# Optimization experiments

Measured on AMD Instinct MI355X. Metric: run time of the kernel, lower is better.

The kernel has to match this reference:

```python
import jax, jax.numpy as jnp
import numpy as np

N = 200_000          # nodes
E = 6_400_000        # edges (avg degree 32)
U, T, C, G = 200_000, 20_000, 5_000, 10_000  # table sizes
DU, DT, DC, DG = 8, 8, 2, 8                  # embedding dims
IC, H, OC = 8, 16, 1                          # input/hidden/output channels


def setup_inputs() -> dict:
    key = jax.random.key(0)
    ks = jax.random.split(key, 24)
    # node type in {0,1,2,4}
    tcode = jnp.array([0, 1, 2, 4], dtype=jnp.int32)[jax.random.randint(ks[0], (N,), 0, 4)]
    # per-type in-range index (size lookup by type code; slot 3 unused)
    sizes = jnp.array([U, T, C, 1, G], dtype=jnp.float32)
    u = jax.random.uniform(ks[1], (N,))
    idx = jnp.floor(u * sizes[tcode]).astype(jnp.int32)
    known = jax.random.randint(ks[2], (N,), 0, 2).astype(jnp.int32)
    features = jnp.stack([idx, known, tcode], axis=1)  # [N, 3]
    edges = jax.random.randint(ks[3], (2, E), 0, N).astype(jnp.int32)
    label_masks = jax.random.randint(ks[4], (N,), 0, 2).astype(jnp.int32)

    def w(k, shape, s=0.1):
        return jax.random.normal(k, shape, dtype=jnp.float32) * s

    return {
        "edges": edges, "features": features, "label_masks": label_masks,
        "user_emb": w(ks[5], (U, DU)), "known_emb": w(ks[6], (2, DU)),
        "mask_emb": w(ks[7], (2, DU)), "cat_emb": w(ks[8], (C, DC)),
        "topic_emb": w(ks[9], (T, DT)), "group_emb": w(ks[10], (G, DG)),
        "user_W": w(ks[11], (DU, IC)), "user_b": jnp.zeros((IC,), jnp.float32),
        "mask_W": w(ks[12], (DU, IC)), "mask_b": jnp.zeros((IC,), jnp.float32),
        "cat_W": w(ks[13], (DC, IC)), "cat_b": jnp.zeros((IC,), jnp.float32),
        "topic_W": w(ks[14], (DT, IC)), "topic_b": jnp.zeros((IC,), jnp.float32),
        "group_W": w(ks[15], (DG, IC)), "group_b": jnp.zeros((IC,), jnp.float32),
        "W0": w(ks[16], (IC, H)), "b0": jnp.zeros((H,), jnp.float32),
        "W2": w(ks[17], (H, OC)), "b2": jnp.zeros((OC,), jnp.float32),
    }


def _assemble(features, label_masks, user_emb, known_emb, mask_emb, cat_emb,
              topic_emb, group_emb, user_W, user_b, mask_W, mask_b, cat_W, cat_b,
              topic_W, topic_b, group_W, group_b):
    idx, known, tcode = features[:, 0], features[:, 1], features[:, 2]
    relu = jax.nn.relu
    # proj = Sequential(ReLU, Linear): relu first, then linear
    user_f = relu(user_emb[jnp.clip(idx, 0, U - 1)] + known_emb[jnp.clip(known, 0, 1)]) @ user_W + user_b
    topic_f = relu(topic_emb[jnp.clip(idx, 0, T - 1)]) @ topic_W + topic_b
    cat_f = relu(cat_emb[jnp.clip(idx, 0, C - 1)]) @ cat_W + cat_b
    group_f = relu(group_emb[jnp.clip(idx, 0, G - 1)]) @ group_W + group_b
    t = tcode[:, None]
    x = jnp.where(t == 0, user_f,
        jnp.where(t == 1, topic_f,
        jnp.where(t == 2, cat_f,
        jnp.where(t == 4, group_f, 0.0))))
    mask_f = jax.nn.sigmoid(relu(mask_emb[label_masks]) @ mask_W + mask_b)
    return x * mask_f  # [N, IC]


def _gcn_norm(edges, n):
    # add self-loops, symmetric normalization (PyG GCNConv default)
    loops = jnp.arange(n, dtype=edges.dtype)
    row = jnp.concatenate([edges[0], loops])
    col = jnp.concatenate([edges[1], loops])
    deg = jax.ops.segment_sum(jnp.ones_like(col, dtype=jnp.float32), col, num_segments=n)
    dis = jnp.where(deg > 0, jax.lax.rsqrt(jnp.where(deg > 0, deg, 1.0)), 0.0)
    return row, col, dis[row] * dis[col]


def _gcn_conv(x, row, col, norm, W, b):
    h = x @ W                                   # [N, out]
    msg = norm[:, None] * h[row]                # gather + scale over edges
    out = jax.ops.segment_sum(msg, col, num_segments=x.shape[0])
    return out + b


def reference(edges, features, label_masks, user_emb, known_emb, mask_emb,
              cat_emb, topic_emb, group_emb, user_W, user_b, mask_W, mask_b,
              cat_W, cat_b, topic_W, topic_b, group_W, group_b, W0, b0, W2, b2):
    x = _assemble(features, label_masks, user_emb, known_emb, mask_emb, cat_emb,
                  topic_emb, group_emb, user_W, user_b, mask_W, mask_b, cat_W,
                  cat_b, topic_W, topic_b, group_W, group_b)
    row, col, norm = _gcn_norm(edges, x.shape[0])
    # Original forward applies layers[0] (relu) then layers[-1]; layers[1] is skipped.
    x = jax.nn.relu(_gcn_conv(x, row, col, norm, W0, b0))
    return _gcn_conv(x, row, col, norm, W2, b2)  # [N, 1]
```

## Files before the change

### kernel.cpp

```cpp
#include <hip/hip_runtime.h>
#include <math.h>

constexpr int NN = 200000;
constexpr int EE = 6400000;
constexpr int NB = (NN + 255) / 256;
constexpr int U_ = 200000, T_ = 20000, C_ = 5000, G_ = 10000;

constexpr int BSH2  = 9;
constexpr int BUCKN = 1 << BSH2;
constexpr int NBUCK = (NN + BUCKN - 1) / BUCKN;
constexpr int CAP   = 18432;
constexpr int CHUNK  = 8192;
constexpr int NCHUNK = (EE + CHUNK - 1) / CHUNK;
constexpr int PER    = (NCHUNK + 255) / 256;

__device__ __forceinline__ int clampi(int v, int lo, int hi){ return v < lo ? lo : (v > hi ? hi : v); }
__device__ __forceinline__ float reluf(float v){ return v > 0.f ? v : 0.f; }


__global__ __launch_bounds__(512) void k_hist(const int* __restrict__ edges,
                                              int* __restrict__ cntmat){
  __shared__ int h[NBUCK];
  int t = threadIdx.x;
  for (int i = t; i < NBUCK; i += 512) h[i] = 0;
  __syncthreads();
  int base = blockIdx.x * CHUNK;
  int n = min(CHUNK, EE - base);
  for (int k = t; k < n; k += 512)
    atomicAdd(&h[edges[EE + base + k] >> BSH2], 1);
  __syncthreads();
  for (int i = t; i < NBUCK; i += 512)
    cntmat[(size_t)blockIdx.x * NBUCK + i] = h[i];
}


__global__ void k_scan2(const int* __restrict__ cntmat, int* __restrict__ offT,
                        int* __restrict__ binCnt){
  __shared__ int sc[256];
  int t = threadIdx.x;
  int b = blockIdx.x;
  int v[PER];
  int loc = 0;
  #pragma unroll
  for (int j = 0; j < PER; j++){
    int c = t * PER + j;
    v[j] = (c < NCHUNK) ? cntmat[(size_t)c * NBUCK + b] : 0;
    loc += v[j];
  }
  sc[t] = loc; __syncthreads();
  for (int d = 1; d < 256; d <<= 1){
    int u = (t >= d) ? sc[t - d] : 0;
    __syncthreads();
    sc[t] += u;
    __syncthreads();
  }
  int run = b * CAP + sc[t] - loc;
  #pragma unroll
  for (int j = 0; j < PER; j++){
    int c = t * PER + j;
    if (c < NCHUNK){ offT[(size_t)b * NCHUNK + c] = run; run += v[j]; }
  }
  if (t == 255) binCnt[b] = sc[255];
}


__global__ __launch_bounds__(512) void k_binA3(const int* __restrict__ edges,
                                               const int* __restrict__ cntmat,
                                               const int* __restrict__ offT,
                                               int* __restrict__ bin){
  __shared__ int cur[NBUCK];
  __shared__ int dlt[NBUCK];
  __shared__ int wsum[8];
  __shared__ int stage[CHUNK];
  __shared__ unsigned short stageB[CHUNK];

  int t = threadIdx.x;
  int chunk = blockIdx.x;
  int my = (t < NBUCK) ? cntmat[(size_t)chunk * NBUCK + t] : 0;
  int lane = t & 63, wid = t >> 6;
  int incl = my;
  #pragma unroll
  for (int d = 1; d < 64; d <<= 1){
    int u = __shfl_up(incl, d);
    if (lane >= d) incl += u;
  }
  if (lane == 63) wsum[wid] = incl;
  __syncthreads();
  int wpre = 0;
  #pragma unroll
  for (int w = 0; w < 8; w++) wpre += (w < wid) ? wsum[w] : 0;
  int excl = wpre + incl - my;
  if (t < NBUCK){
    cur[t] = excl;
    dlt[t] = offT[(size_t)t * NCHUNK + chunk] - excl;
  }
  __syncthreads();
  int base = chunk * CHUNK;
  int n = min(CHUNK, EE - base);
  for (int k = t; k < n; k += 512){
    int c = edges[EE + base + k];
    int r = edges[base + k];
    int b = c >> BSH2;
    int p = atomicAdd(&cur[b], 1);
    stage[p]  = r | ((c & (BUCKN - 1)) << 18);
    stageB[p] = (unsigned short)b;
  }
  __syncthreads();
  for (int k = t; k < n; k += 512){
    int b = stageB[k];
    int addr = dlt[b] + k;
    if (addr < (b + 1) * CAP)
      bin[addr] = stage[k];
  }
}


__global__ __launch_bounds__(512) void k_binB2(
    const int* __restrict__ bin, const int* __restrict__ binCnt,
    int* __restrict__ off, int* __restrict__ deg, int* __restrict__ seg,
    double* __restrict__ dis, int* __restrict__ srow){
  __shared__ int hist[4 * BUCKN];
  __shared__ int sc[512];
  int t = threadIdx.x;
  int b = blockIdx.x;
  int nb = b << BSH2;
  int nloc = min(BUCKN, NN - nb);
  int s0 = b * CAP;
  int s1 = s0 + min(binCnt[b], CAP);

  hist[t] = 0; hist[t + 512] = 0; hist[t + 1024] = 0; hist[t + 1536] = 0;
  __syncthreads();
  for (int k = s0 + t; k < s1; k += 512){
    int w = bin[k];
    int key = ((w >> 18) << 2) | ((w & 0x3FFFF) >> 16);
    atomicAdd(&hist[key], 1);
  }
  __syncthreads();
  int h0 = hist[4*t], h1 = hist[4*t+1], h2 = hist[4*t+2], h3 = hist[4*t+3];
  int tot = h0 + h1 + h2 + h3;
  sc[t] = tot; __syncthreads();
  for (int d = 1; d < 512; d <<= 1){
    int u = (t >= d) ? sc[t - d] : 0;
    __syncthreads();
    sc[t] += u;
    __syncthreads();
  }
  int base = sc[t] - tot;
  if (t < nloc){
    off[nb + t] = s0 + base;
    deg[nb + t] = tot;
    seg[nb + t] = h0 | ((h0 + h1) << 10) | ((h0 + h1 + h2) << 20);
    dis[nb + t] = 1.0 / sqrt((double)(tot + 1));
  }
  __syncthreads();
  hist[4*t]     = base;
  hist[4*t + 1] = base + h0;
  hist[4*t + 2] = base + h0 + h1;
  hist[4*t + 3] = base + h0 + h1 + h2;
  __syncthreads();
  for (int k = s0 + t; k < s1; k += 512){
    int w = bin[k];
    int key = ((w >> 18) << 2) | ((w & 0x3FFFF) >> 16);
    int p = atomicAdd(&hist[key], 1);
    srow[s0 + p] = w & 0x3FFFF;
  }
}


__global__ void k_assemble(
    const int* __restrict__ features, const int* __restrict__ lmask,
    const float* __restrict__ user_emb, const float* __restrict__ known_emb,
    const float* __restrict__ mask_emb, const float* __restrict__ cat_emb,
    const float* __restrict__ topic_emb, const float* __restrict__ group_emb,
    const float* __restrict__ user_W, const float* __restrict__ user_b,
    const float* __restrict__ mask_W, const float* __restrict__ mask_b,
    const float* __restrict__ cat_W, const float* __restrict__ cat_b,
    const float* __restrict__ topic_W, const float* __restrict__ topic_b,
    const float* __restrict__ group_W, const float* __restrict__ group_b,
    const double* __restrict__ dis, float* __restrict__ xs1)
{
  __shared__ float s_userW[64], s_topicW[64], s_groupW[64], s_maskW[64];
  __shared__ float s_catW[16], s_knownE[16], s_maskE[16];
  __shared__ float s_userb[8], s_topicb[8], s_catb[8], s_groupb[8], s_maskb[8];
  int tid = threadIdx.x;
  if (tid < 64){ s_userW[tid]=user_W[tid]; s_topicW[tid]=topic_W[tid];
                 s_groupW[tid]=group_W[tid]; s_maskW[tid]=mask_W[tid]; }
  if (tid < 16){ s_catW[tid]=cat_W[tid]; s_knownE[tid]=known_emb[tid]; s_maskE[tid]=mask_emb[tid]; }
  if (tid < 8){ s_userb[tid]=user_b[tid]; s_topicb[tid]=topic_b[tid]; s_catb[tid]=cat_b[tid];
                s_groupb[tid]=group_b[tid]; s_maskb[tid]=mask_b[tid]; }
  __syncthreads();

  int i = blockIdx.x * 256 + tid;
  if (i >= NN) return;

  int idx   = features[3*i + 0];
  int known = features[3*i + 1];
  int tc    = features[3*i + 2];

  double x[8];
  #pragma unroll
  for (int k = 0; k < 8; k++) x[k] = 0.0;

  if (tc == 0){
    int id = clampi(idx, 0, U_-1);
    int kn = clampi(known, 0, 1);
    float a[8];
    #pragma unroll
    for (int d = 0; d < 8; d++) a[d] = reluf(user_emb[(size_t)id*8 + d] + s_knownE[kn*8 + d]);
    #pragma unroll
    for (int k = 0; k < 8; k++){
      double s = (double)s_userb[k];
      #pragma unroll
      for (int d = 0; d < 8; d++) s += (double)a[d] * (double)s_userW[d*8 + k];
      x[k] = s;
    }
  } else if (tc == 1){
    int id = clampi(idx, 0, T_-1);
    float a[8];
    #pragma unroll
    for (int d = 0; d < 8; d++) a[d] = reluf(topic_emb[(size_t)id*8 + d]);
    #pragma unroll
    for (int k = 0; k < 8; k++){
      double s = (double)s_topicb[k];
      #pragma unroll
      for (int d = 0; d < 8; d++) s += (double)a[d] * (double)s_topicW[d*8 + k];
      x[k] = s;
    }
  } else if (tc == 2){
    int id = clampi(idx, 0, C_-1);
    float a0 = reluf(cat_emb[(size_t)id*2 + 0]);
    float a1 = reluf(cat_emb[(size_t)id*2 + 1]);
    #pragma unroll
    for (int k = 0; k < 8; k++)
      x[k] = (double)s_catb[k] + (double)a0*(double)s_catW[k] + (double)a1*(double)s_catW[8 + k];
  } else if (tc == 4){
    int id = clampi(idx, 0, G_-1);
    float a[8];
    #pragma unroll
    for (int d = 0; d < 8; d++) a[d] = reluf(group_emb[(size_t)id*8 + d]);
    #pragma unroll
    for (int k = 0; k < 8; k++){
      double s = (double)s_groupb[k];
      #pragma unroll
      for (int d = 0; d < 8; d++) s += (double)a[d] * (double)s_groupW[d*8 + k];
      x[k] = s;
    }
  }

  int m = clampi(lmask[i], 0, 1);
  float me[8];
  #pragma unroll
  for (int d = 0; d < 8; d++) me[d] = reluf(s_maskE[m*8 + d]);
  double di = dis[i];
  float xo[8];
  #pragma unroll
  for (int k = 0; k < 8; k++){
    double s = (double)s_maskb[k];
    #pragma unroll
    for (int d = 0; d < 8; d++) s += (double)me[d] * (double)s_maskW[d*8 + k];
    double mf = 1.0 / (1.0 + exp(-s));
    xo[k] = (float)(di * x[k] * mf);
  }
  float4* xp = (float4*)(xs1 + (size_t)i * 8);
  xp[0] = make_float4(xo[0], xo[1], xo[2], xo[3]);
  xp[1] = make_float4(xo[4], xo[5], xo[6], xo[7]);
}


__global__ void k_agg1(const float* __restrict__ xs1, const int* __restrict__ srow,
                       const int* __restrict__ off, const int* __restrict__ cnt,
                       const int* __restrict__ seg, const double* __restrict__ dis,
                       const float* __restrict__ b0, const float* __restrict__ W0,
                       const float* __restrict__ W2, float* __restrict__ h2s)
{
  __shared__ float sW0[128], sb0[16], sW2[16];
  int tid = threadIdx.x;
  if (tid < 128) sW0[tid] = W0[tid];
  if (tid < 16){ sb0[tid] = b0[tid]; sW2[tid] = W2[tid]; }
  __syncthreads();

  int gid = blockIdx.x * 256 + tid;
  int i = gid >> 1, h = gid & 1;
  if (i >= NN) return;

  const float4* xp = (const float4*)xs1;
  float4 sv = xp[(size_t)i*2 + h];
  double a0 = sv.x, a1 = sv.y, a2 = sv.z, a3 = sv.w;
  int s = off[i], c = cnt[i], sg = seg[i];
  int bnd[5];
  bnd[0] = 0;
  bnd[1] = sg & 1023;
  bnd[2] = (sg >> 10) & 1023;
  bnd[3] = (sg >> 20) & 1023;
  bnd[4] = c;
  #pragma unroll 1
  for (int p = 0; p < 4; p++){
    int j = bnd[p], je = bnd[p + 1];
    for (; j + 4 <= je; j += 4){
      int r0 = srow[s+j], r1 = srow[s+j+1], r2 = srow[s+j+2], r3 = srow[s+j+3];
      float4 v0 = xp[(size_t)r0*2 + h], v1 = xp[(size_t)r1*2 + h],
             v2 = xp[(size_t)r2*2 + h], v3 = xp[(size_t)r3*2 + h];
      a0 += v0.x; a1 += v0.y; a2 += v0.z; a3 += v0.w;
      a0 += v1.x; a1 += v1.y; a2 += v1.z; a3 += v1.w;
      a0 += v2.x; a1 += v2.y; a2 += v2.z; a3 += v2.w;
      a0 += v3.x; a1 += v3.y; a2 += v3.z; a3 += v3.w;
    }
    for (; j < je; ++j){
      int r = srow[s + j];
      float4 v = xp[(size_t)r*2 + h];
      a0 += v.x; a1 += v.y; a2 += v.z; a3 += v.w;
    }
  }
  double e0 = __shfl_xor(a0, 1), e1 = __shfl_xor(a1, 1),
         e2 = __shfl_xor(a2, 1), e3 = __shfl_xor(a3, 1);
  double X[8];
  if (h == 0){ X[0]=a0; X[1]=a1; X[2]=a2; X[3]=a3; X[4]=e0; X[5]=e1; X[6]=e2; X[7]=e3; }
  else       { X[0]=e0; X[1]=e1; X[2]=e2; X[3]=e3; X[4]=a0; X[5]=a1; X[6]=a2; X[7]=a3; }

  double di = dis[i];
  double h2p = 0.0;
  #pragma unroll
  for (int jj = 0; jj < 8; jj++){
    int j = h * 8 + jj;
    double t = 0.0;
    #pragma unroll
    for (int cc = 0; cc < 8; cc++) t += X[cc] * (double)sW0[cc*16 + j];
    t = di * t + (double)sb0[j];
    double x2 = t > 0.0 ? t : 0.0;
    h2p += x2 * (double)sW2[j];
  }
  double h2 = h2p + __shfl_xor(h2p, 1);
  if (h == 0) h2s[i] = (float)(di * h2);
}


__global__ void k_agg2(const float* __restrict__ h2s, const int* __restrict__ srow,
                       const int* __restrict__ off, const int* __restrict__ cnt,
                       const double* __restrict__ dis, const float* __restrict__ b2,
                       float* __restrict__ out)
{
  int gid = blockIdx.x * 256 + threadIdx.x;
  int i = gid >> 1, h = gid & 1;
  if (i >= NN) return;
  double acc = (h == 0) ? (double)h2s[i] : 0.0;
  int s = off[i], c = cnt[i];
  for (int j = h; j < c; j += 2)
    acc += (double)h2s[srow[s + j]];
  acc += __shfl_xor(acc, 1);
  if (h == 0) out[i] = (float)(dis[i] * acc + (double)b2[0]);
}


extern "C" void kernel_launch(void* const* d_in, const int* in_sizes, int n_in,
                              void* d_out, int out_size, void* d_ws, size_t ws_size,
                              hipStream_t stream)
{
  const int*   edges      = (const int*)  d_in[0];
  const int*   features   = (const int*)  d_in[1];
  const int*   label_mask = (const int*)  d_in[2];
  const float* user_emb   = (const float*)d_in[3];
  const float* known_emb  = (const float*)d_in[4];
  const float* mask_emb   = (const float*)d_in[5];
  const float* cat_emb    = (const float*)d_in[6];
  const float* topic_emb  = (const float*)d_in[7];
  const float* group_emb  = (const float*)d_in[8];
  const float* user_W     = (const float*)d_in[9];
  const float* user_b     = (const float*)d_in[10];
  const float* mask_W     = (const float*)d_in[11];
  const float* mask_b     = (const float*)d_in[12];
  const float* cat_W      = (const float*)d_in[13];
  const float* cat_b      = (const float*)d_in[14];
  const float* topic_W    = (const float*)d_in[15];
  const float* topic_b    = (const float*)d_in[16];
  const float* group_W    = (const float*)d_in[17];
  const float* group_b    = (const float*)d_in[18];
  const float* W0         = (const float*)d_in[19];
  const float* b0         = (const float*)d_in[20];
  const float* W2         = (const float*)d_in[21];
  const float* b2         = (const float*)d_in[22];
  float* out = (float*)d_out;

  char* ws = (char*)d_ws;
  size_t o = 0;
  auto alloc = [&](size_t bytes){ void* p = ws + o; o += (bytes + 255) & ~255ull; return p; };
  int*    cntmat = (int*)   alloc((size_t)NCHUNK * NBUCK * 4);
  int*    offT   = (int*)   alloc((size_t)NBUCK * NCHUNK * 4);
  int*    binCnt = (int*)   alloc((size_t)NBUCK * 4);
  int*    off    = (int*)   alloc((size_t)NN * 4);
  int*    deg    = (int*)   alloc((size_t)NN * 4);
  int*    seg    = (int*)   alloc((size_t)NN * 4);
  double* dis    = (double*)alloc((size_t)NN * 8);
  int*    srow   = (int*)   alloc((size_t)NBUCK * CAP * 4);
  int*    bin    = (int*)   alloc((size_t)NBUCK * CAP * 4);
  float*  xs1    = (float*) alloc((size_t)NN * 8 * 4);
  float*  h2s    = (float*) alloc((size_t)NN * 4);

  k_hist    <<<NCHUNK, 512, 0, stream>>>(edges, cntmat);
  k_scan2   <<<NBUCK,  256, 0, stream>>>(cntmat, offT, binCnt);
  k_binA3   <<<NCHUNK, 512, 0, stream>>>(edges, cntmat, offT, bin);
  k_binB2   <<<NBUCK,  512, 0, stream>>>(bin, binCnt, off, deg, seg, dis, srow);
  k_assemble<<<NB,     256, 0, stream>>>(features, label_mask,
      user_emb, known_emb, mask_emb, cat_emb, topic_emb, group_emb,
      user_W, user_b, mask_W, mask_b, cat_W, cat_b,
      topic_W, topic_b, group_W, group_b, dis, xs1);
  k_agg1    <<<(2*NN + 255)/256, 256, 0, stream>>>(xs1, srow, off, deg, seg, dis, b0, W0, W2, h2s);
  k_agg2    <<<(2*NN + 255)/256, 256, 0, stream>>>(h2s, srow, off, deg, dis, b2, out);
}
```

Baseline: 224.1 us.

## Split node aggregation across four lanes and stage sorted rows in LDS

The first and second aggregation kernels now give each node four lanes instead of two. In the first kernel each lane gathers a float2 slice of the 8-wide feature, and the full feature is rebuilt with two rounds of xor shuffles. In the second kernel the neighbour sum is strided by four. Separately, the bucket sort kernel now scatters sorted row ids into a shared-memory stage and writes them to global memory contiguously, instead of scattering them directly. The aim is more memory parallelism in the gather-bound kernels and coalesced srow writes. The cost is more threads, extra shuffles, narrower loads per edge, and a large LDS footprint (about 72KB) that may reduce occupancy of the sort kernel.

Measured after the change: 185.0 us. 17.4% less time.

```diff
diff --git a/kernel.cpp b/kernel.cpp
--- a/kernel.cpp
+++ b/kernel.cpp
@@ -121,12 +121,14 @@
     double* __restrict__ dis, int* __restrict__ srow){
   __shared__ int hist[4 * BUCKN];
   __shared__ int sc[512];
+  __shared__ int stage[CAP];
   int t = threadIdx.x;
   int b = blockIdx.x;
   int nb = b << BSH2;
   int nloc = min(BUCKN, NN - nb);
   int s0 = b * CAP;
-  int s1 = s0 + min(binCnt[b], CAP);
+  int cntb = min(binCnt[b], CAP);
+  int s1 = s0 + cntb;
 
   hist[t] = 0; hist[t + 512] = 0; hist[t + 1024] = 0; hist[t + 1536] = 0;
   __syncthreads();
@@ -162,8 +164,11 @@
     int w = bin[k];
     int key = ((w >> 18) << 2) | ((w & 0x3FFFF) >> 16);
     int p = atomicAdd(&hist[key], 1);
-    srow[s0 + p] = w & 0x3FFFF;
-  }
+    stage[p] = w & 0x3FFFF;
+  }
+  __syncthreads();
+  for (int k = t; k < cntb; k += 512)
+    srow[s0 + k] = stage[k];
 }
 
 
@@ -280,12 +285,12 @@
   __syncthreads();
 
   int gid = blockIdx.x * 256 + tid;
-  int i = gid >> 1, h = gid & 1;
+  int i = gid >> 2, h = gid & 3;
   if (i >= NN) return;
 
-  const float4* xp = (const float4*)xs1;
-  float4 sv = xp[(size_t)i*2 + h];
-  double a0 = sv.x, a1 = sv.y, a2 = sv.z, a3 = sv.w;
+  const float2* xp = (const float2*)xs1;
+  float2 sv = xp[(size_t)i*4 + h];
+  double a0 = sv.x, a1 = sv.y;
   int s = off[i], c = cnt[i], sg = seg[i];
   int bnd[5];
   bnd[0] = 0;
@@ -298,30 +303,34 @@
     int j = bnd[p], je = bnd[p + 1];
     for (; j + 4 <= je; j += 4){
       int r0 = srow[s+j], r1 = srow[s+j+1], r2 = srow[s+j+2], r3 = srow[s+j+3];
-      float4 v0 = xp[(size_t)r0*2 + h], v1 = xp[(size_t)r1*2 + h],
-             v2 = xp[(size_t)r2*2 + h], v3 = xp[(size_t)r3*2 + h];
-      a0 += v0.x; a1 += v0.y; a2 += v0.z; a3 += v0.w;
-      a0 += v1.x; a1 += v1.y; a2 += v1.z; a3 += v1.w;
-      a0 += v2.x; a1 += v2.y; a2 += v2.z; a3 += v2.w;
-      a0 += v3.x; a1 += v3.y; a2 += v3.z; a3 += v3.w;
+      float2 v0 = xp[(size_t)r0*4 + h], v1 = xp[(size_t)r1*4 + h],
+             v2 = xp[(size_t)r2*4 + h], v3 = xp[(size_t)r3*4 + h];
+      a0 += v0.x; a1 += v0.y;
+      a0 += v1.x; a1 += v1.y;
+      a0 += v2.x; a1 += v2.y;
+      a0 += v3.x; a1 += v3.y;
     }
     for (; j < je; ++j){
       int r = srow[s + j];
-      float4 v = xp[(size_t)r*2 + h];
-      a0 += v.x; a1 += v.y; a2 += v.z; a3 += v.w;
+      float2 v = xp[(size_t)r*4 + h];
+      a0 += v.x; a1 += v.y;
     }
   }
-  double e0 = __shfl_xor(a0, 1), e1 = __shfl_xor(a1, 1),
-         e2 = __shfl_xor(a2, 1), e3 = __shfl_xor(a3, 1);
+  double e0 = __shfl_xor(a0, 1), e1 = __shfl_xor(a1, 1);
+  double q0, q1, q2, q3;
+  if ((h & 1) == 0){ q0 = a0; q1 = a1; q2 = e0; q3 = e1; }
+  else             { q0 = e0; q1 = e1; q2 = a0; q3 = a1; }
+  double f0 = __shfl_xor(q0, 2), f1 = __shfl_xor(q1, 2),
+         f2 = __shfl_xor(q2, 2), f3 = __shfl_xor(q3, 2);
   double X[8];
-  if (h == 0){ X[0]=a0; X[1]=a1; X[2]=a2; X[3]=a3; X[4]=e0; X[5]=e1; X[6]=e2; X[7]=e3; }
-  else       { X[0]=e0; X[1]=e1; X[2]=e2; X[3]=e3; X[4]=a0; X[5]=a1; X[6]=a2; X[7]=a3; }
+  if ((h & 2) == 0){ X[0]=q0; X[1]=q1; X[2]=q2; X[3]=q3; X[4]=f0; X[5]=f1; X[6]=f2; X[7]=f3; }
+  else             { X[0]=f0; X[1]=f1; X[2]=f2; X[3]=f3; X[4]=q0; X[5]=q1; X[6]=q2; X[7]=q3; }
 
   double di = dis[i];
   double h2p = 0.0;
   #pragma unroll
-  for (int jj = 0; jj < 8; jj++){
-    int j = h * 8 + jj;
+  for (int jj = 0; jj < 4; jj++){
+    int j = h * 4 + jj;
     double t = 0.0;
     #pragma unroll
     for (int cc = 0; cc < 8; cc++) t += X[cc] * (double)sW0[cc*16 + j];
@@ -329,8 +338,9 @@
     double x2 = t > 0.0 ? t : 0.0;
     h2p += x2 * (double)sW2[j];
   }
-  double h2 = h2p + __shfl_xor(h2p, 1);
-  if (h == 0) h2s[i] = (float)(di * h2);
+  h2p += __shfl_xor(h2p, 1);
+  h2p += __shfl_xor(h2p, 2);
+  if (h == 0) h2s[i] = (float)(di * h2p);
 }
 
 
@@ -340,13 +350,14 @@
                        float* __restrict__ out)
 {
   int gid = blockIdx.x * 256 + threadIdx.x;
-  int i = gid >> 1, h = gid & 1;
+  int i = gid >> 2, h = gid & 3;
   if (i >= NN) return;
   double acc = (h == 0) ? (double)h2s[i] : 0.0;
   int s = off[i], c = cnt[i];
-  for (int j = h; j < c; j += 2)
+  for (int j = h; j < c; j += 4)
     acc += (double)h2s[srow[s + j]];
   acc += __shfl_xor(acc, 1);
+  acc += __shfl_xor(acc, 2);
   if (h == 0) out[i] = (float)(dis[i] * acc + (double)b2[0]);
 }
 
@@ -403,6 +414,6 @@
       user_emb, known_emb, mask_emb, cat_emb, topic_emb, group_emb,
       user_W, user_b, mask_W, mask_b, cat_W, cat_b,
       topic_W, topic_b, group_W, group_b, dis, xs1);
-  k_agg1    <<<(2*NN + 255)/256, 256, 0, stream>>>(xs1, srow, off, deg, seg, dis, b0, W0, W2, h2s);
-  k_agg2    <<<(2*NN + 255)/256, 256, 0, stream>>>(h2s, srow, off, deg, dis, b2, out);
-}
+  k_agg1    <<<(4*NN + 255)/256, 256, 0, stream>>>(xs1, srow, off, deg, seg, dis, b0, W0, W2, h2s);
+  k_agg2    <<<(4*NN + 255)/256, 256, 0, stream>>>(h2s, srow, off, deg, dis, b2, out);
+}
```
